# Performance work log

Hardware: AMD Instinct MI355X
Metric: run time of the kernel (lower is better)

Reference implementation:

```python
import jax, jax.numpy as jnp
import numpy as np


def setup_inputs() -> dict:
    key = jax.random.key(0)
    heatmaps = jax.random.normal(key, (16, 24, 64, 64, 64), dtype=jnp.float32)
    return {"heatmaps": heatmaps}


def reference(heatmaps) -> jnp.ndarray:
    N, J, D, H, W = heatmaps.shape
    # softmax over the flattened D*H*W volume per (n, j)
    p = jax.nn.softmax(heatmaps.reshape(N, J, D * H * W), axis=2).reshape(N, J, D, H, W)
    x_maps = p.sum(axis=(2, 3))  # (N, J, W)
    y_maps = p.sum(axis=(2, 4))  # (N, J, H)
    z_maps = p.sum(axis=(3, 4))  # (N, J, D)
    w_idx = jnp.arange(W, dtype=p.dtype)
    h_idx = jnp.arange(H, dtype=p.dtype)
    d_idx = jnp.arange(D, dtype=p.dtype)
    x_preds = (x_maps * w_idx).sum(axis=2) / W - 0.5
    y_preds = (y_maps * h_idx).sum(axis=2) / H - 0.5
    z_preds = (z_maps * d_idx).sum(axis=2) / D - 0.5
    return jnp.stack((x_preds, y_preds, z_preds), axis=2)  # (N, J, 3)
```

## Files before the change

kernel.cpp:

```cpp
#include <hip/hip_runtime.h>


#define NJ     384
#define VOL    262144
#define CHUNKS 32
#define BLOCK  256
#define EPB    (VOL / CHUNKS)
#define ITERS  (EPB / 4 / BLOCK)

typedef float vfloat4 __attribute__((ext_vector_type(4)));

__global__ __launch_bounds__(BLOCK) void jir_accum(const float* __restrict__ hm,
                                                   float4* __restrict__ partial) {
    const int slice = blockIdx.x >> 5;
    const int chunk = blockIdx.x & 31;
    const int t = threadIdx.x;

    const vfloat4* __restrict__ base =
        (const vfloat4*)(hm + (size_t)slice * VOL + (size_t)chunk * EPB) + t;

    const float w0    = (float)((t & 15) << 2);
    const float hbase = (float)(t >> 4);
    const float dbase = (float)(chunk << 1);

    float S = 0.f, Sx = 0.f, Sy = 0.f, Sz = 0.f;

#pragma unroll
    for (int i = 0; i < ITERS; ++i) {
        const vfloat4 q = __builtin_nontemporal_load(base + i * BLOCK);
        const float e0 = __expf(q.x);
        const float e1 = __expf(q.y);
        const float e2 = __expf(q.z);
        const float e3 = __expf(q.w);
        const float Se = (e0 + e1) + (e2 + e3);
        const float hh = hbase + (float)((i & 3) << 4);
        const float dd = dbase + (float)(i >> 2);
        const float cx = fmaf(3.0f, e3, fmaf(2.0f, e2, e1));
        S  += Se;
        Sx += fmaf(w0, Se, cx);
        Sy  = fmaf(hh, Se, Sy);
        Sz  = fmaf(dd, Se, Sz);
    }

#pragma unroll
    for (int off = 32; off > 0; off >>= 1) {
        S  += __shfl_down(S,  off, 64);
        Sx += __shfl_down(Sx, off, 64);
        Sy += __shfl_down(Sy, off, 64);
        Sz += __shfl_down(Sz, off, 64);
    }

    __shared__ float red[BLOCK / 64][4];
    const int wid  = t >> 6;
    const int lane = t & 63;
    if (lane == 0) {
        red[wid][0] = S; red[wid][1] = Sx; red[wid][2] = Sy; red[wid][3] = Sz;
    }
    __syncthreads();
    if (t == 0) {
        float4 p;
        p.x = (red[0][0] + red[1][0]) + (red[2][0] + red[3][0]);
        p.y = (red[0][1] + red[1][1]) + (red[2][1] + red[3][1]);
        p.z = (red[0][2] + red[1][2]) + (red[2][2] + red[3][2]);
        p.w = (red[0][3] + red[1][3]) + (red[2][3] + red[3][3]);
        partial[blockIdx.x] = p;
    }
}

__global__ void jir_finalize(const float4* __restrict__ partial,
                             float* __restrict__ out) {
    const int s = blockIdx.x * blockDim.x + threadIdx.x;
    if (s < NJ) {
        float S = 0.f, Sx = 0.f, Sy = 0.f, Sz = 0.f;
#pragma unroll
        for (int c = 0; c < CHUNKS; ++c) {
            const float4 p = partial[s * CHUNKS + c];
            S += p.x; Sx += p.y; Sy += p.z; Sz += p.w;
        }
        const float scale = 1.0f / (S * 64.0f);
        out[s * 3 + 0] = Sx * scale - 0.5f;
        out[s * 3 + 1] = Sy * scale - 0.5f;
        out[s * 3 + 2] = Sz * scale - 0.5f;
    }
}

extern "C" void kernel_launch(void* const* d_in, const int* in_sizes, int n_in,
                              void* d_out, int out_size, void* d_ws, size_t ws_size,
                              hipStream_t stream) {
    const float* hm = (const float*)d_in[0];
    float* out = (float*)d_out;
    float4* partial = (float4*)d_ws;

    jir_accum<<<NJ * CHUNKS, BLOCK, 0, stream>>>(hm, partial);
    jir_finalize<<<2, 192, 0, stream>>>(partial, out);
}
```

Baseline: 486.4 us.

## Fuse finalize into one block-per-slice kernel with 512 threads

Replaces the two-kernel scheme (32 chunk blocks per slice writing partials, then a finalize kernel) with one 512-thread block per (n, j) slice. That block does the full reduction and writes the three coordinates directly. The change also pulls the w0*Se multiply out of the inner loop by keeping a separate Cx sum and applying w0*S once at the end. It removes the second launch and the partials round trip. In exchange the grid drops to 384 blocks, which may leave too few waves in flight to keep HBM busy and may spread work unevenly across the CUs.

```diff
diff --git a/kernel.cpp b/kernel.cpp
--- a/kernel.cpp
+++ b/kernel.cpp
@@ -1,31 +1,26 @@
 #include <hip/hip_runtime.h>
 
 
-#define NJ     384
-#define VOL    262144
-#define CHUNKS 32
-#define BLOCK  256
-#define EPB    (VOL / CHUNKS)
-#define ITERS  (EPB / 4 / BLOCK)
+#define NJ    384
+#define VOL   262144
+#define BLOCK 512
+#define ITERS (VOL / 4 / BLOCK)
 
 typedef float vfloat4 __attribute__((ext_vector_type(4)));
 
-__global__ __launch_bounds__(BLOCK) void jir_accum(const float* __restrict__ hm,
-                                                   float4* __restrict__ partial) {
-    const int slice = blockIdx.x >> 5;
-    const int chunk = blockIdx.x & 31;
+__global__ __launch_bounds__(BLOCK) void jir_fused(const float* __restrict__ hm,
+                                                   float* __restrict__ out) {
+    const int s = blockIdx.x;
     const int t = threadIdx.x;
 
-    const vfloat4* __restrict__ base =
-        (const vfloat4*)(hm + (size_t)slice * VOL + (size_t)chunk * EPB) + t;
+    const vfloat4* __restrict__ base = (const vfloat4*)(hm + (size_t)s * VOL) + t;
 
     const float w0    = (float)((t & 15) << 2);
     const float hbase = (float)(t >> 4);
-    const float dbase = (float)(chunk << 1);
 
-    float S = 0.f, Sx = 0.f, Sy = 0.f, Sz = 0.f;
+    float S = 0.f, Cx = 0.f, Sy = 0.f, Sz = 0.f;
 
-#pragma unroll
+#pragma unroll 8
     for (int i = 0; i < ITERS; ++i) {
         const vfloat4 q = __builtin_nontemporal_load(base + i * BLOCK);
         const float e0 = __expf(q.x);
@@ -33,14 +28,15 @@
         const float e2 = __expf(q.z);
         const float e3 = __expf(q.w);
         const float Se = (e0 + e1) + (e2 + e3);
-        const float hh = hbase + (float)((i & 3) << 4);
-        const float dd = dbase + (float)(i >> 2);
+        const float hh = hbase + (float)((i & 1) << 5);
+        const float dd = (float)(i >> 1);
         const float cx = fmaf(3.0f, e3, fmaf(2.0f, e2, e1));
         S  += Se;
-        Sx += fmaf(w0, Se, cx);
+        Cx += cx;
         Sy  = fmaf(hh, Se, Sy);
         Sz  = fmaf(dd, Se, Sz);
     }
+    float Sx = fmaf(w0, S, Cx);
 
 #pragma unroll
     for (int off = 32; off > 0; off >>= 1) {
@@ -57,30 +53,26 @@
         red[wid][0] = S; red[wid][1] = Sx; red[wid][2] = Sy; red[wid][3] = Sz;
     }
     __syncthreads();
-    if (t == 0) {
-        float4 p;
-        p.x = (red[0][0] + red[1][0]) + (red[2][0] + red[3][0]);
-        p.y = (red[0][1] + red[1][1]) + (red[2][1] + red[3][1]);
-        p.z = (red[0][2] + red[1][2]) + (red[2][2] + red[3][2]);
-        p.w = (red[0][3] + red[1][3]) + (red[2][3] + red[3][3]);
-        partial[blockIdx.x] = p;
-    }
-}
 
-__global__ void jir_finalize(const float4* __restrict__ partial,
-                             float* __restrict__ out) {
-    const int s = blockIdx.x * blockDim.x + threadIdx.x;
-    if (s < NJ) {
-        float S = 0.f, Sx = 0.f, Sy = 0.f, Sz = 0.f;
+    if (t < 64) {
+        const int nw = BLOCK / 64;
+        float a0 = (t < nw) ? red[t][0] : 0.f;
+        float a1 = (t < nw) ? red[t][1] : 0.f;
+        float a2 = (t < nw) ? red[t][2] : 0.f;
+        float a3 = (t < nw) ? red[t][3] : 0.f;
 #pragma unroll
-        for (int c = 0; c < CHUNKS; ++c) {
-            const float4 p = partial[s * CHUNKS + c];
-            S += p.x; Sx += p.y; Sy += p.z; Sz += p.w;
+        for (int off = 4; off > 0; off >>= 1) {
+            a0 += __shfl_down(a0, off, 64);
+            a1 += __shfl_down(a1, off, 64);
+            a2 += __shfl_down(a2, off, 64);
+            a3 += __shfl_down(a3, off, 64);
         }
-        const float scale = 1.0f / (S * 64.0f);
-        out[s * 3 + 0] = Sx * scale - 0.5f;
-        out[s * 3 + 1] = Sy * scale - 0.5f;
-        out[s * 3 + 2] = Sz * scale - 0.5f;
+        if (t == 0) {
+            const float scale = 1.0f / (a0 * 64.0f);
+            out[s * 3 + 0] = a1 * scale - 0.5f;
+            out[s * 3 + 1] = a2 * scale - 0.5f;
+            out[s * 3 + 2] = a3 * scale - 0.5f;
+        }
     }
 }
 
@@ -89,8 +81,7 @@
                               hipStream_t stream) {
     const float* hm = (const float*)d_in[0];
     float* out = (float*)d_out;
-    float4* partial = (float4*)d_ws;
+    (void)d_ws; (void)ws_size;
 
-    jir_accum<<<NJ * CHUNKS, BLOCK, 0, stream>>>(hm, partial);
-    jir_finalize<<<2, 192, 0, stream>>>(partial, out);
+    jir_fused<<<NJ, BLOCK, 0, stream>>>(hm, out);
 }
```

After: 485.1 us. No clear change (-0.3%).
